# Optimization experiments

Hardware: AMD Instinct MI355X
Metric: run time of the kernel (lower is better)

Reference implementation:

```python
import jax, jax.numpy as jnp
import numpy as np

B, S, H = 1, 2048, 2048
NH, NKV, DH = 8, 1, 256
ROPE_THETA = 10000.0
SCALE = DH ** -0.5
NEG = -1e9


def setup_inputs() -> dict:
    key = jax.random.key(0)
    k1, k2, k3, k4, k5 = jax.random.split(key, 5)
    x = jax.random.normal(k1, (B, S, H), dtype=jnp.float32)
    position_ids = jnp.broadcast_to(jnp.arange(S, dtype=jnp.int32)[None, :], (B, S))
    causal = jnp.tril(jnp.ones((S, S), dtype=bool))
    attention_mask = jnp.where(causal, 0.0, NEG).astype(jnp.float32)[None, None]  # [1,1,S,S]
    std = 0.02
    w_q = jax.random.normal(k2, (H, NH * DH), dtype=jnp.float32) * std
    w_k = jax.random.normal(k3, (H, NKV * DH), dtype=jnp.float32) * std
    w_v = jax.random.normal(k4, (H, NKV * DH), dtype=jnp.float32) * std
    w_o = jax.random.normal(k5, (NH * DH, H), dtype=jnp.float32) * std
    return {"x": x, "position_ids": position_ids, "attention_mask": attention_mask,
            "w_q": w_q, "w_k": w_k, "w_v": w_v, "w_o": w_o}


def _rope_cos_sin(position_ids):
    # inv_freq: [DH/2]
    inv_freq = 1.0 / (ROPE_THETA ** (jnp.arange(0, DH, 2, dtype=jnp.float32) / DH))
    freqs = position_ids.astype(jnp.float32)[:, :, None] * inv_freq[None, None, :]  # [B,S,DH/2]
    emb = jnp.concatenate([freqs, freqs], axis=-1)  # [B,S,DH]
    return jnp.cos(emb), jnp.sin(emb)


def _rotate_half(t):
    t1, t2 = jnp.split(t, 2, axis=-1)
    return jnp.concatenate([-t2, t1], axis=-1)


def reference(x, position_ids, attention_mask, w_q, w_k, w_v, w_o):
    b, s, _ = x.shape
    g = NH // NKV  # kv group size
    q = (x @ w_q).reshape(b, s, NH, DH).transpose(0, 2, 1, 3)   # [b,nh,s,d]
    k = (x @ w_k).reshape(b, s, NKV, DH).transpose(0, 2, 1, 3)  # [b,nkv,s,d]
    v = (x @ w_v).reshape(b, s, NKV, DH).transpose(0, 2, 1, 3)
    cos, sin = _rope_cos_sin(position_ids)
    cos, sin = cos[:, None], sin[:, None]  # broadcast over heads
    q = q * cos + _rotate_half(q) * sin
    k = k * cos + _rotate_half(k) * sin
    # GQA: view q as [b,nkv,g,s,d]; equivalent to repeat_kv without materializing
    qg = q.reshape(b, NKV, g, s, DH)
    scores = jnp.einsum('bkgid,bkjd->bkgij', qg, k) * SCALE      # [b,nkv,g,s,s]
    scores = scores + attention_mask[:, :, None, :, :]
    attn = jax.nn.softmax(scores.astype(jnp.float32), axis=-1).astype(q.dtype)
    out = jnp.einsum('bkgij,bkjd->bkgid', attn, v)               # [b,nkv,g,s,d]
    out = out.reshape(b, NH, s, DH).transpose(0, 2, 1, 3).reshape(b, s, NH * DH)
    out = out @ w_o
    return out, attn.reshape(b, NH, s, s)
```

## Files before the change

kernel.cpp:

```cpp
#include <hip/hip_runtime.h>
#include <hip/hip_bf16.h>
#include <hip/hip_fp16.h>

typedef float f32x4 __attribute__((ext_vector_type(4)));
typedef _Float16 half8 __attribute__((ext_vector_type(8)));
typedef unsigned short u16;
typedef unsigned short u16x8 __attribute__((ext_vector_type(8)));

#define DEVI __device__ __forceinline__

DEVI void async_cp16(void* lds, const void* g) {
  __builtin_amdgcn_global_load_lds(
      (const __attribute__((address_space(1))) void*)g,
      (__attribute__((address_space(3))) void*)lds,
      16, 0, 0);
}

DEVI u16 f2h(float x) {
  union { _Float16 h; u16 u; } v;
  v.h = (_Float16)x;
  return v.u;
}

__global__ __launch_bounds__(256)
void k_prep(const float* __restrict__ x, const float* __restrict__ wq,
            const float* __restrict__ wk, const float* __restrict__ wv,
            const float* __restrict__ wo,
            u16* __restrict__ xb, u16* __restrict__ wqkvT, u16* __restrict__ woT) {
  int bx = blockIdx.x;
  if (bx >= 72) {
    size_t base = ((size_t)(bx - 72) * 32 + blockIdx.y) * 2048 + threadIdx.x * 8;
    float4 v0 = *(const float4*)(x + base);
    float4 v1 = *(const float4*)(x + base + 4);
    ushort4 o0, o1;
    o0.x = f2h(v0.x); o0.y = f2h(v0.y); o0.z = f2h(v0.z); o0.w = f2h(v0.w);
    o1.x = f2h(v1.x); o1.y = f2h(v1.y); o1.z = f2h(v1.z); o1.w = f2h(v1.w);
    *(ushort4*)(xb + base) = o0;
    *(ushort4*)(xb + base + 4) = o1;
    return;
  }
  __shared__ u16 tile[64][65];
  const float* in; int ldin, rowoff, cx; u16* out;
  if (bx < 32)      { in = wq; ldin = 2048; out = wqkvT; rowoff = 0;    cx = bx; }
  else if (bx < 36) { in = wk; ldin = 256;  out = wqkvT; rowoff = 2048; cx = bx - 32; }
  else if (bx < 40) { in = wv; ldin = 256;  out = wqkvT; rowoff = 2304; cx = bx - 36; }
  else              { in = wo; ldin = 2048; out = woT;   rowoff = 0;    cx = bx - 40; }
  int r0 = blockIdx.y * 64, c0 = cx * 64;
  int tx = threadIdx.x & 63, ty = threadIdx.x >> 6;
  for (int rr = ty; rr < 64; rr += 4)
    tile[rr][tx] = f2h(in[(size_t)(r0 + rr) * ldin + (c0 + tx)]);
  __syncthreads();
  for (int rr = ty; rr < 64; rr += 4)
    out[(size_t)(c0 + rr + rowoff) * 2048 + (r0 + tx)] = tile[tx][rr];
}

__global__ __launch_bounds__(256, 2)
void k_gemmQKV(const u16* __restrict__ A, const u16* __restrict__ B,
               const int* __restrict__ pos,
               u16* __restrict__ qh, u16* __restrict__ kh, u16* __restrict__ vT) {
  const int lda = 2048, ldb = 2048;
  const int id = blockIdx.x;
  const int xcd = id & 7, t = id >> 3;
  const int cx = t % 10;
  const int mt = xcd + 8 * (t / 10);
  const int i0 = mt * 64, j0 = cx * 256;

  __shared__ __align__(16) char shm[81920];
  const int tid = threadIdx.x;
  const int wave = tid >> 6, lane = tid & 63;
  const int wn = wave * 64;
  const int quad = lane >> 4, r = lane & 15;

  f32x4 acc[4][4] = {};

  const int srow = tid >> 3;
  const int scol = ((((tid & 7) << 4)) ^ (((tid >> 3) & 7) << 4)) >> 1;
  const u16* gA = A + (size_t)(i0 + srow) * lda + scol;
  const u16* gB = B + (size_t)(j0 + srow) * ldb + scol;
  const int cswz = (quad * 16) ^ ((r & 7) << 4);
  const int nk = 2048 >> 6;

#pragma unroll
  for (int c = 0; c < 2; c++)
    async_cp16(shm + tid * 16 + c * 4096, gA + (size_t)(c * 32) * lda);
#pragma unroll
  for (int c = 0; c < 8; c++)
    async_cp16(shm + 16384 + tid * 16 + c * 4096, gB + (size_t)(c * 32) * ldb);

  for (int kt = 0; kt < nk; kt++) {
    const int cur = kt & 1;
    __builtin_amdgcn_sched_barrier(0);
    asm volatile("s_waitcnt vmcnt(0)" ::: "memory");
    __builtin_amdgcn_s_barrier();
    __builtin_amdgcn_sched_barrier(0);
    if (kt + 1 < nk) {
      const int nxt = cur ^ 1;
      const u16* a1 = gA + (size_t)(kt + 1) * 64;
      const u16* b1 = gB + (size_t)(kt + 1) * 64;
#pragma unroll
      for (int c = 0; c < 2; c++)
        async_cp16(shm + nxt * 8192 + tid * 16 + c * 4096, a1 + (size_t)(c * 32) * lda);
#pragma unroll
      for (int c = 0; c < 8; c++)
        async_cp16(shm + 16384 + nxt * 32768 + tid * 16 + c * 4096, b1 + (size_t)(c * 32) * ldb);
    }
    const char* bufA = shm + cur * 8192;
    const char* bufB = shm + 16384 + cur * 32768;
#pragma unroll
    for (int kh = 0; kh < 2; kh++) {
      const int inrow = cswz ^ (kh * 64);
      half8 af[4], bf[4];
#pragma unroll
      for (int mm = 0; mm < 4; mm++)
        af[mm] = *(const half8*)(bufA + (mm * 16 + r) * 128 + inrow);
#pragma unroll
      for (int n = 0; n < 4; n++)
        bf[n] = *(const half8*)(bufB + (wn + n * 16 + r) * 128 + inrow);
      __builtin_amdgcn_s_setprio(1);
#pragma unroll
      for (int mm = 0; mm < 4; mm++)
#pragma unroll
        for (int n = 0; n < 4; n++)
          acc[mm][n] = __builtin_amdgcn_mfma_f32_16x16x32_f16(af[mm], bf[n], acc[mm][n], 0, 0, 0);
      __builtin_amdgcn_s_setprio(0);
    }
  }

  __syncthreads();
  float* T = (float*)shm;
#pragma unroll
  for (int mm = 0; mm < 4; mm++) {
    int row = mm * 16 + quad * 4;
#pragma unroll
    for (int n = 0; n < 4; n++) {
      int col = wn + n * 16 + r;
#pragma unroll
      for (int v = 0; v < 4; v++) T[(row + v) * 260 + col] = acc[mm][n][v];
    }
  }
  __syncthreads();

  if (cx < 9) {
    const int trow = tid >> 2, tc = tid & 3;
    const int s = i0 + trow;
    u16* dst = (cx < 8) ? (qh + (size_t)s * 2048 + cx * 256) : (kh + (size_t)s * 256);
    const float p = (float)pos[s];
#pragma unroll
    for (int k = 0; k < 4; k++) {
      const int ib = tc * 8 + k * 32;
      u16x8 lo, hi;
#pragma unroll
      for (int e = 0; e < 8; e++) {
        int i = ib + e;
        float fr = __expf((float)i * (-9.210340371976184f / 128.0f)) * p;
        float sn, cs;
        sincosf(fr, &sn, &cs);
        float a = T[trow * 260 + i];
        float b = T[trow * 260 + i + 128];
        lo[e] = f2h(a * cs - b * sn);
        hi[e] = f2h(b * cs + a * sn);
      }
      *(u16x8*)(dst + ib) = lo;
      *(u16x8*)(dst + ib + 128) = hi;
    }
  } else {
    u16* dst = vT + (size_t)tid * 2048 + i0;
#pragma unroll
    for (int c = 0; c < 8; c++) {
      u16x8 w;
#pragma unroll
      for (int e = 0; e < 8; e++) w[e] = f2h(T[(c * 8 + e) * 260 + tid]);
      *(u16x8*)(dst + c * 8) = w;
    }
  }
}

__global__ __launch_bounds__(256, 3)
void k_gemm(const u16* __restrict__ A, int lda,
            const u16* __restrict__ B, int ldb,
            float* __restrict__ C, int ldc, int nN, int K) {
  const int id = blockIdx.x;
  const int xcd = id & 7, t = id >> 3;
  const int by = t % nN;
  const int mt = xcd + 8 * (t / nN);
  const int i0 = mt * 64, j0 = by * 128;

  __shared__ __align__(16) u16 As[2][64 * 64];
  __shared__ __align__(16) u16 Bs[2][128 * 64];
  const int tid = threadIdx.x;
  const int wave = tid >> 6, lane = tid & 63;
  const int wm = (wave >> 1) * 32, wn = (wave & 1) * 64;
  const int quad = lane >> 4, r = lane & 15;

  f32x4 acc[2][4] = {};

  const int srow = tid >> 3;
  const int scol = ((((tid & 7) << 4)) ^ (((tid >> 3) & 7) << 4)) >> 1;
  const u16* gA = A + (size_t)(i0 + srow) * lda + scol;
  const u16* gB = B + (size_t)(j0 + srow) * ldb + scol;
  const int cswz = (quad * 16) ^ ((r & 7) << 4);
  const int nk = K >> 6;

#pragma unroll
  for (int c = 0; c < 2; c++)
    async_cp16((u16*)As[0] + tid * 8 + c * 2048, gA + (size_t)(c * 32) * lda);
#pragma unroll
  for (int c = 0; c < 4; c++)
    async_cp16((u16*)Bs[0] + tid * 8 + c * 2048, gB + (size_t)(c * 32) * ldb);

  for (int kt = 0; kt < nk; kt++) {
    const int cur = kt & 1;
    __builtin_amdgcn_sched_barrier(0);
    asm volatile("s_waitcnt vmcnt(0)" ::: "memory");
    __builtin_amdgcn_s_barrier();
    __builtin_amdgcn_sched_barrier(0);
    if (kt + 1 < nk) {
      const u16* a1 = gA + (size_t)(kt + 1) * 64;
      const u16* b1 = gB + (size_t)(kt + 1) * 64;
#pragma unroll
      for (int c = 0; c < 2; c++)
        async_cp16((u16*)As[cur ^ 1] + tid * 8 + c * 2048, a1 + (size_t)(c * 32) * lda);
#pragma unroll
      for (int c = 0; c < 4; c++)
        async_cp16((u16*)Bs[cur ^ 1] + tid * 8 + c * 2048, b1 + (size_t)(c * 32) * ldb);
    }
    const char* bufA = (const char*)As[cur];
    const char* bufB = (const char*)Bs[cur];
#pragma unroll
    for (int kh = 0; kh < 2; kh++) {
      const int inrow = cswz ^ (kh * 64);
      half8 af[2], bf[4];
#pragma unroll
      for (int mm = 0; mm < 2; mm++)
        af[mm] = *(const half8*)(bufA + (wm + mm * 16 + r) * 128 + inrow);
#pragma unroll
      for (int n = 0; n < 4; n++)
        bf[n] = *(const half8*)(bufB + (wn + n * 16 + r) * 128 + inrow);
      __builtin_amdgcn_s_setprio(1);
#pragma unroll
      for (int mm = 0; mm < 2; mm++)
#pragma unroll
        for (int n = 0; n < 4; n++)
          acc[mm][n] = __builtin_amdgcn_mfma_f32_16x16x32_f16(af[mm], bf[n], acc[mm][n], 0, 0, 0);
      __builtin_amdgcn_s_setprio(0);
    }
  }

#pragma unroll
  for (int mm = 0; mm < 2; mm++) {
    int row = i0 + wm + mm * 16 + quad * 4;
#pragma unroll
    for (int n = 0; n < 4; n++) {
      int col = j0 + wn + n * 16 + r;
      float* cp = C + (size_t)row * ldc + col;
#pragma unroll
      for (int v = 0; v < 4; v++) cp[(size_t)v * ldc] = acc[mm][n][v];
    }
  }
}

__global__ __launch_bounds__(256)
void k_scores(const u16* __restrict__ qh, const u16* __restrict__ kh,
              float* __restrict__ attn, float* __restrict__ lsum) {
  int id = blockIdx.x;
  int ti = (int)((sqrtf(8.0f * (float)id + 1.0f) - 1.0f) * 0.5f);
  while ((ti + 1) * (ti + 2) / 2 <= id) ti++;
  while (ti * (ti + 1) / 2 > id) ti--;
  int tj = id - ti * (ti + 1) / 2;
  const int i0 = ti * 128, j0 = tj * 128;
  const int h = blockIdx.y;
  const int tid = threadIdx.x;
  float* outb = attn + ((size_t)h << 22);

  const u16* A = qh + h * 256;
  __shared__ __align__(16) u16 As[2][128 * 32];
  __shared__ __align__(16) u16 Bs[2][128 * 32];
  __shared__ float psum[128];
  const int wave = tid >> 6, lane = tid & 63;
  const int wm = (wave >> 1) * 64, wn = (wave & 1) * 64;
  const int quad = lane >> 4, r = lane & 15;

  f32x4 acc[4][4] = {};

  const int ar = tid >> 2, ac = (tid & 3) * 8;
  const u16* ag0 = A + (size_t)(i0 + ar) * 2048 + ac;
  const u16* ag1 = ag0 + (size_t)64 * 2048;
  const u16* bg0 = kh + (size_t)(j0 + ar) * 256 + ac;
  const u16* bg1 = bg0 + (size_t)64 * 256;
  const int l0 = tid * 8, l1 = (tid + 256) * 8;

  async_cp16(As[0] + l0, ag0); async_cp16(As[0] + l1, ag1);
  async_cp16(Bs[0] + l0, bg0); async_cp16(Bs[0] + l1, bg1);
  ag0 += 32; ag1 += 32; bg0 += 32; bg1 += 32;
  __syncthreads();

  for (int kt = 0; kt < 8; kt += 2) {
#pragma unroll
    for (int half = 0; half < 2; half++) {
      int cur = half, nxt = half ^ 1;
      if (kt + half + 1 < 8) {
        async_cp16(As[nxt] + l0, ag0); async_cp16(As[nxt] + l1, ag1);
        async_cp16(Bs[nxt] + l0, bg0); async_cp16(Bs[nxt] + l1, bg1);
        ag0 += 32; ag1 += 32; bg0 += 32; bg1 += 32;
      }
      half8 af[4], bf[4];
#pragma unroll
      for (int t = 0; t < 4; t++) af[t] = *(const half8*)(As[cur] + (wm + t * 16 + r) * 32 + quad * 8);
#pragma unroll
      for (int t = 0; t < 4; t++) bf[t] = *(const half8*)(Bs[cur] + (wn + t * 16 + r) * 32 + quad * 8);
#pragma unroll
      for (int ta = 0; ta < 4; ta++)
#pragma unroll
        for (int tb = 0; tb < 4; tb++)
          acc[ta][tb] = __builtin_amdgcn_mfma_f32_16x16x32_f16(af[ta], bf[tb], acc[ta][tb], 0, 0, 0);
      __syncthreads();
    }
  }

  if (tid < 128) psum[tid] = 0.f;
  __syncthreads();
#pragma unroll
  for (int ta = 0; ta < 4; ta++) {
#pragma unroll
    for (int v = 0; v < 4; v++) {
      int row = i0 + wm + ta * 16 + quad * 4 + v;
      float rs = 0.f;
#pragma unroll
      for (int tb = 0; tb < 4; tb++) {
        int col = j0 + wn + tb * 16 + r;
        float val = (col <= row) ? __expf(acc[ta][tb][v] * 0.0625f) : 0.0f;
        outb[(size_t)row * 2048 + col] = val;
        rs += val;
      }
      rs += __shfl_xor(rs, 1); rs += __shfl_xor(rs, 2);
      rs += __shfl_xor(rs, 4); rs += __shfl_xor(rs, 8);
      if (r == 0) atomicAdd(&psum[wm + ta * 16 + quad * 4 + v], rs);
    }
  }
  __syncthreads();
  if (tid < 128)
    lsum[((size_t)h * 2048 + i0 + tid) * 16 + tj] = psum[tid];
}

__global__ __launch_bounds__(256)
void k_pv(float* __restrict__ attn, const u16* __restrict__ vT,
          const float* __restrict__ lsum, u16* __restrict__ o) {
  const int h = blockIdx.y;
  const int i0 = (63 - blockIdx.x) * 32;
  float* Ab = attn + ((size_t)h << 22);
  const int kmax = i0 + 32;
  __shared__ __align__(16) u16 As[2][32 * 64];
  __shared__ __align__(16) u16 Bs[2][256 * 64];
  __shared__ float inv_l[32];
  const int tid = threadIdx.x;
  const int wave = tid >> 6, lane = tid & 63;
  const int wn = wave * 64;
  const int quad = lane >> 4, r = lane & 15;

  if (tid < 32) {
    int i = i0 + tid;
    const float* lp = lsum + ((size_t)h * 2048 + i) * 16;
    int nt = (i >> 7) + 1;
    float s = 0.f;
    for (int t = 0; t < nt; t++) s += lp[t];
    inv_l[tid] = 1.0f / s;
  }
  __syncthreads();

  const int arr = tid >> 3, ac8 = (tid & 7) * 8;
  const int aso = arr * 64 + ((((tid & 7) * 16) ^ ((arr & 7) << 4)) >> 1);
  float* agp = Ab + (size_t)(i0 + arr) * 2048 + ac8;
  const float ainv = inv_l[arr];
  const int brow = tid >> 3;
  const int bcol = ((((tid & 7) * 16)) ^ (((tid >> 3) & 7) << 4)) >> 1;
  const u16* bg = vT + (size_t)brow * 2048 + bcol;
  const int cswz = (quad * 16) ^ ((r & 7) << 4);

  f32x4 acc[2][4] = {};

#define PV_STAGE(buf, k0)                                                        \
  {                                                                              \
    _Pragma("unroll")                                                            \
    for (int c = 0; c < 8; c++)                                                  \
      async_cp16((u16*)Bs[buf] + tid * 8 + c * 2048,                             \
                 bg + (size_t)(c * 32) * 2048 + (k0));                           \
    float4 v0 = *(const float4*)(agp + (k0));                                    \
    float4 v1 = *(const float4*)(agp + (k0) + 4);                                \
    v0.x *= ainv; v0.y *= ainv; v0.z *= ainv; v0.w *= ainv;                      \
    v1.x *= ainv; v1.y *= ainv; v1.z *= ainv; v1.w *= ainv;                      \
    *(float4*)(agp + (k0)) = v0;                                                 \
    *(float4*)(agp + (k0) + 4) = v1;                                             \
    u16x8 w;                                                                     \
    w[0] = f2h(v0.x); w[1] = f2h(v0.y); w[2] = f2h(v0.z); w[3] = f2h(v0.w);      \
    w[4] = f2h(v1.x); w[5] = f2h(v1.y); w[6] = f2h(v1.z); w[7] = f2h(v1.w);      \
    *(u16x8*)((u16*)As[buf] + aso) = w;                                          \
  }

  PV_STAGE(0, 0);
  const int nkt = (kmax + 63) >> 6;
  for (int kt = 0; kt < nkt; kt++) {
    const int cur = kt & 1;
    __syncthreads();
    if (kt + 1 < nkt) PV_STAGE(cur ^ 1, (kt + 1) * 64);
    const char* bA = (const char*)As[cur];
    const char* bB = (const char*)Bs[cur];
#pragma unroll
    for (int kh = 0; kh < 2; kh++) {
      const int inrow = cswz ^ (kh * 64);
      half8 af[2], bf[4];
#pragma unroll
      for (int ta = 0; ta < 2; ta++)
        af[ta] = *(const half8*)(bA + (ta * 16 + r) * 128 + inrow);
#pragma unroll
      for (int tb = 0; tb < 4; tb++)
        bf[tb] = *(const half8*)(bB + (wn + tb * 16 + r) * 128 + inrow);
#pragma unroll
      for (int ta = 0; ta < 2; ta++)
#pragma unroll
        for (int tb = 0; tb < 4; tb++)
          acc[ta][tb] = __builtin_amdgcn_mfma_f32_16x16x32_f16(af[ta], bf[tb], acc[ta][tb], 0, 0, 0);
    }
  }
#pragma unroll
  for (int ta = 0; ta < 2; ta++) {
    int row = i0 + ta * 16 + quad * 4;
#pragma unroll
    for (int tb = 0; tb < 4; tb++) {
      int col = h * 256 + wn + tb * 16 + r;
#pragma unroll
      for (int v = 0; v < 4; v++)
        o[(size_t)(row + v) * 2048 + col] = f2h(acc[ta][tb][v]);
    }
  }
}

extern "C" void kernel_launch(void* const* d_in, const int* in_sizes, int n_in,
                              void* d_out, int out_size, void* d_ws, size_t ws_size,
                              hipStream_t stream) {
  const float* x   = (const float*)d_in[0];
  const int*   pos = (const int*)d_in[1];
  const float* w_q = (const float*)d_in[3];
  const float* w_k = (const float*)d_in[4];
  const float* w_v = (const float*)d_in[5];
  const float* w_o = (const float*)d_in[6];

  float* out  = (float*)d_out;
  float* attn = out + (size_t)2048 * 2048;

  char* ws = (char*)d_ws;
  u16*   xb    = (u16*)ws;
  u16*   wqkvT = xb + (size_t)2048 * 2048;
  u16*   woT   = wqkvT + (size_t)2560 * 2048;
  u16*   qh    = woT + (size_t)2048 * 2048;
  u16*   kh    = qh + (size_t)2048 * 2048;
  u16*   vT    = kh + (size_t)2048 * 256;
  u16*   ob    = vT + (size_t)256 * 2048;
  float* lsum  = (float*)(ob + (size_t)2048 * 2048);

  k_prep<<<dim3(136, 32), 256, 0, stream>>>(x, w_q, w_k, w_v, w_o, xb, wqkvT, woT);

  k_gemmQKV<<<dim3(320), 256, 0, stream>>>(xb, wqkvT, pos, qh, kh, vT);

  k_scores<<<dim3(136, 8), 256, 0, stream>>>(qh, kh, attn, lsum);
  k_pv<<<dim3(64, 8), 256, 0, stream>>>(attn, vT, lsum, ob);

  k_gemm<<<dim3(512), 256, 0, stream>>>(ob, 2048, woT, 2048, out, 2048, 16, 2048);
}
```

Baseline: 326.8 us.

## Fuse scores and PV into one attention kernel keeping probabilities in LDS

Replaces the separate scores kernel (which wrote unnormalised exp to the fp32 attn buffer and partial row sums) and the PV kernel (which re-read, normalised and rewrote attn) with a single kernel per 16-row strip. Each block computes QK^T for its row strip, stores fp16 exponentials in a swizzled 64KB LDS buffer, reduces row sums, then does PV from LDS while writing the normalised attn once. This removes the global round trip of the attention matrix and the lsum buffer. In exchange it uses a fixed exp offset instead of a max subtraction, stores probabilities in fp16, gives small 16-row tiles with K/V loaded directly from global without LDS staging, and the large LDS use limits occupancy.

```diff
diff --git a/kernel.cpp b/kernel.cpp
--- a/kernel.cpp
+++ b/kernel.cpp
@@ -20,6 +20,12 @@
   union { _Float16 h; u16 u; } v;
   v.h = (_Float16)x;
   return v.u;
+}
+
+DEVI float h2f(u16 x) {
+  union { u16 u; _Float16 h; } v;
+  v.u = x;
+  return (float)v.h;
 }
 
 __global__ __launch_bounds__(256)
@@ -107,8 +113,8 @@
     const char* bufA = shm + cur * 8192;
     const char* bufB = shm + 16384 + cur * 32768;
 #pragma unroll
-    for (int kh = 0; kh < 2; kh++) {
-      const int inrow = cswz ^ (kh * 64);
+    for (int kh2 = 0; kh2 < 2; kh2++) {
+      const int inrow = cswz ^ (kh2 * 64);
       half8 af[4], bf[4];
 #pragma unroll
       for (int mm = 0; mm < 4; mm++)
@@ -227,8 +233,8 @@
     const char* bufA = (const char*)As[cur];
     const char* bufB = (const char*)Bs[cur];
 #pragma unroll
-    for (int kh = 0; kh < 2; kh++) {
-      const int inrow = cswz ^ (kh * 64);
+    for (int kh2 = 0; kh2 < 2; kh2++) {
+      const int inrow = cswz ^ (kh2 * 64);
       half8 af[2], bf[4];
 #pragma unroll
       for (int mm = 0; mm < 2; mm++)
@@ -259,177 +265,113 @@
   }
 }
 
-__global__ __launch_bounds__(256)
-void k_scores(const u16* __restrict__ qh, const u16* __restrict__ kh,
-              float* __restrict__ attn, float* __restrict__ lsum) {
-  int id = blockIdx.x;
-  int ti = (int)((sqrtf(8.0f * (float)id + 1.0f) - 1.0f) * 0.5f);
-  while ((ti + 1) * (ti + 2) / 2 <= id) ti++;
-  while (ti * (ti + 1) / 2 > id) ti--;
-  int tj = id - ti * (ti + 1) / 2;
-  const int i0 = ti * 128, j0 = tj * 128;
+__global__ __launch_bounds__(256, 2)
+void k_attn(const u16* __restrict__ qh, const u16* __restrict__ kh,
+            const u16* __restrict__ vT,
+            float* __restrict__ attn, u16* __restrict__ o) {
   const int h = blockIdx.y;
+  const int i0 = (127 - blockIdx.x) * 16;
+  const int kmax = i0 + 16;
+  const int ntiles = (kmax + 127) >> 7;
+
+  __shared__ __align__(16) u16 S16[16 * 2048];
+  __shared__ float rowsum[16];
+  __shared__ float inv_l[16];
+
   const int tid = threadIdx.x;
-  float* outb = attn + ((size_t)h << 22);
-
-  const u16* A = qh + h * 256;
-  __shared__ __align__(16) u16 As[2][128 * 32];
-  __shared__ __align__(16) u16 Bs[2][128 * 32];
-  __shared__ float psum[128];
   const int wave = tid >> 6, lane = tid & 63;
-  const int wm = (wave >> 1) * 64, wn = (wave & 1) * 64;
   const int quad = lane >> 4, r = lane & 15;
 
-  f32x4 acc[4][4] = {};
-
-  const int ar = tid >> 2, ac = (tid & 3) * 8;
-  const u16* ag0 = A + (size_t)(i0 + ar) * 2048 + ac;
-  const u16* ag1 = ag0 + (size_t)64 * 2048;
-  const u16* bg0 = kh + (size_t)(j0 + ar) * 256 + ac;
-  const u16* bg1 = bg0 + (size_t)64 * 256;
-  const int l0 = tid * 8, l1 = (tid + 256) * 8;
-
-  async_cp16(As[0] + l0, ag0); async_cp16(As[0] + l1, ag1);
-  async_cp16(Bs[0] + l0, bg0); async_cp16(Bs[0] + l1, bg1);
-  ag0 += 32; ag1 += 32; bg0 += 32; bg1 += 32;
-  __syncthreads();
-
-  for (int kt = 0; kt < 8; kt += 2) {
-#pragma unroll
-    for (int half = 0; half < 2; half++) {
-      int cur = half, nxt = half ^ 1;
-      if (kt + half + 1 < 8) {
-        async_cp16(As[nxt] + l0, ag0); async_cp16(As[nxt] + l1, ag1);
-        async_cp16(Bs[nxt] + l0, bg0); async_cp16(Bs[nxt] + l1, bg1);
-        ag0 += 32; ag1 += 32; bg0 += 32; bg1 += 32;
-      }
-      half8 af[4], bf[4];
-#pragma unroll
-      for (int t = 0; t < 4; t++) af[t] = *(const half8*)(As[cur] + (wm + t * 16 + r) * 32 + quad * 8);
-#pragma unroll
-      for (int t = 0; t < 4; t++) bf[t] = *(const half8*)(Bs[cur] + (wn + t * 16 + r) * 32 + quad * 8);
-#pragma unroll
-      for (int ta = 0; ta < 4; ta++)
-#pragma unroll
-        for (int tb = 0; tb < 4; tb++)
-          acc[ta][tb] = __builtin_amdgcn_mfma_f32_16x16x32_f16(af[ta], bf[tb], acc[ta][tb], 0, 0, 0);
-      __syncthreads();
-    }
-  }
-
-  if (tid < 128) psum[tid] = 0.f;
-  __syncthreads();
-#pragma unroll
-  for (int ta = 0; ta < 4; ta++) {
+  const u16* qp = qh + (size_t)(i0 + r) * 2048 + h * 256 + quad * 8;
+  half8 qf[8];
+#pragma unroll
+  for (int kf = 0; kf < 8; kf++) qf[kf] = *(const half8*)(qp + kf * 32);
+
+  if (tid < 16) rowsum[tid] = 0.f;
+  __syncthreads();
+
+  for (int jt = 0; jt < ntiles; jt++) {
+    const int jc = jt * 128 + wave * 32;
+    half8 bf[2][8];
+#pragma unroll
+    for (int nf = 0; nf < 2; nf++) {
+      const u16* kp = kh + (size_t)(jc + nf * 16 + r) * 256 + quad * 8;
+#pragma unroll
+      for (int kf = 0; kf < 8; kf++) bf[nf][kf] = *(const half8*)(kp + kf * 32);
+    }
+    f32x4 acc[2] = {};
+#pragma unroll
+    for (int kf = 0; kf < 8; kf++)
+#pragma unroll
+      for (int nf = 0; nf < 2; nf++)
+        acc[nf] = __builtin_amdgcn_mfma_f32_16x16x32_f16(qf[kf], bf[nf][kf], acc[nf], 0, 0, 0);
 #pragma unroll
     for (int v = 0; v < 4; v++) {
-      int row = i0 + wm + ta * 16 + quad * 4 + v;
+      const int row = quad * 4 + v;
+      const int grow = i0 + row;
       float rs = 0.f;
 #pragma unroll
-      for (int tb = 0; tb < 4; tb++) {
-        int col = j0 + wn + tb * 16 + r;
-        float val = (col <= row) ? __expf(acc[ta][tb][v] * 0.0625f) : 0.0f;
-        outb[(size_t)row * 2048 + col] = val;
-        rs += val;
+      for (int nf = 0; nf < 2; nf++) {
+        const int col = jc + nf * 16 + r;
+        float e = (col <= grow) ? __expf(acc[nf][v] * 0.0625f - 4.0f) : 0.f;
+        u16 eh = f2h(e);
+        rs += h2f(eh);
+        S16[row * 2048 + (col ^ ((row & 7) << 3))] = eh;
       }
       rs += __shfl_xor(rs, 1); rs += __shfl_xor(rs, 2);
       rs += __shfl_xor(rs, 4); rs += __shfl_xor(rs, 8);
-      if (r == 0) atomicAdd(&psum[wm + ta * 16 + quad * 4 + v], rs);
-    }
-  }
-  __syncthreads();
-  if (tid < 128)
-    lsum[((size_t)h * 2048 + i0 + tid) * 16 + tj] = psum[tid];
-}
-
-__global__ __launch_bounds__(256)
-void k_pv(float* __restrict__ attn, const u16* __restrict__ vT,
-          const float* __restrict__ lsum, u16* __restrict__ o) {
-  const int h = blockIdx.y;
-  const int i0 = (63 - blockIdx.x) * 32;
-  float* Ab = attn + ((size_t)h << 22);
-  const int kmax = i0 + 32;
-  __shared__ __align__(16) u16 As[2][32 * 64];
-  __shared__ __align__(16) u16 Bs[2][256 * 64];
-  __shared__ float inv_l[32];
-  const int tid = threadIdx.x;
-  const int wave = tid >> 6, lane = tid & 63;
-  const int wn = wave * 64;
-  const int quad = lane >> 4, r = lane & 15;
-
-  if (tid < 32) {
-    int i = i0 + tid;
-    const float* lp = lsum + ((size_t)h * 2048 + i) * 16;
-    int nt = (i >> 7) + 1;
-    float s = 0.f;
-    for (int t = 0; t < nt; t++) s += lp[t];
-    inv_l[tid] = 1.0f / s;
-  }
-  __syncthreads();
-
-  const int arr = tid >> 3, ac8 = (tid & 7) * 8;
-  const int aso = arr * 64 + ((((tid & 7) * 16) ^ ((arr & 7) << 4)) >> 1);
-  float* agp = Ab + (size_t)(i0 + arr) * 2048 + ac8;
-  const float ainv = inv_l[arr];
-  const int brow = tid >> 3;
-  const int bcol = ((((tid & 7) * 16)) ^ (((tid >> 3) & 7) << 4)) >> 1;
-  const u16* bg = vT + (size_t)brow * 2048 + bcol;
-  const int cswz = (quad * 16) ^ ((r & 7) << 4);
-
-  f32x4 acc[2][4] = {};
-
-#define PV_STAGE(buf, k0)                                                        \
-  {                                                                              \
-    _Pragma("unroll")                                                            \
-    for (int c = 0; c < 8; c++)                                                  \
-      async_cp16((u16*)Bs[buf] + tid * 8 + c * 2048,                             \
-                 bg + (size_t)(c * 32) * 2048 + (k0));                           \
-    float4 v0 = *(const float4*)(agp + (k0));                                    \
-    float4 v1 = *(const float4*)(agp + (k0) + 4);                                \
-    v0.x *= ainv; v0.y *= ainv; v0.z *= ainv; v0.w *= ainv;                      \
-    v1.x *= ainv; v1.y *= ainv; v1.z *= ainv; v1.w *= ainv;                      \
-    *(float4*)(agp + (k0)) = v0;                                                 \
-    *(float4*)(agp + (k0) + 4) = v1;                                             \
-    u16x8 w;                                                                     \
-    w[0] = f2h(v0.x); w[1] = f2h(v0.y); w[2] = f2h(v0.z); w[3] = f2h(v0.w);      \
-    w[4] = f2h(v1.x); w[5] = f2h(v1.y); w[6] = f2h(v1.z); w[7] = f2h(v1.w);      \
-    *(u16x8*)((u16*)As[buf] + aso) = w;                                          \
-  }
-
-  PV_STAGE(0, 0);
-  const int nkt = (kmax + 63) >> 6;
-  for (int kt = 0; kt < nkt; kt++) {
-    const int cur = kt & 1;
-    __syncthreads();
-    if (kt + 1 < nkt) PV_STAGE(cur ^ 1, (kt + 1) * 64);
-    const char* bA = (const char*)As[cur];
-    const char* bB = (const char*)Bs[cur];
-#pragma unroll
-    for (int kh = 0; kh < 2; kh++) {
-      const int inrow = cswz ^ (kh * 64);
-      half8 af[2], bf[4];
-#pragma unroll
-      for (int ta = 0; ta < 2; ta++)
-        af[ta] = *(const half8*)(bA + (ta * 16 + r) * 128 + inrow);
-#pragma unroll
-      for (int tb = 0; tb < 4; tb++)
-        bf[tb] = *(const half8*)(bB + (wn + tb * 16 + r) * 128 + inrow);
-#pragma unroll
-      for (int ta = 0; ta < 2; ta++)
-#pragma unroll
-        for (int tb = 0; tb < 4; tb++)
-          acc[ta][tb] = __builtin_amdgcn_mfma_f32_16x16x32_f16(af[ta], bf[tb], acc[ta][tb], 0, 0, 0);
-    }
-  }
-#pragma unroll
-  for (int ta = 0; ta < 2; ta++) {
-    int row = i0 + ta * 16 + quad * 4;
-#pragma unroll
-    for (int tb = 0; tb < 4; tb++) {
-      int col = h * 256 + wn + tb * 16 + r;
-#pragma unroll
-      for (int v = 0; v < 4; v++)
-        o[(size_t)(row + v) * 2048 + col] = f2h(acc[ta][tb][v]);
+      if (r == 0) atomicAdd(&rowsum[row], rs);
+    }
+  }
+  __syncthreads();
+  if (tid < 16) inv_l[tid] = 1.0f / rowsum[tid];
+  __syncthreads();
+
+  const int d0 = wave * 64;
+  const int arow = tid >> 4, acb = (tid & 15) * 8;
+  const float ail = inv_l[arow];
+  float* ap = attn + ((size_t)h << 22) + (size_t)(i0 + arow) * 2048;
+  const u16* sp = S16 + arow * 2048;
+  const int aswz = (arow & 7) << 3;
+
+  f32x4 oacc[4] = {};
+  for (int jt = 0; jt < ntiles; jt++) {
+    half8 pa[4];
+#pragma unroll
+    for (int kf = 0; kf < 4; kf++) {
+      int j = jt * 128 + kf * 32 + quad * 8;
+      pa[kf] = *(const half8*)(S16 + r * 2048 + (j ^ ((r & 7) << 3)));
+    }
+    half8 vf[4][4];
+#pragma unroll
+    for (int nf = 0; nf < 4; nf++) {
+      const u16* vp = vT + (size_t)(d0 + nf * 16 + r) * 2048 + jt * 128 + quad * 8;
+#pragma unroll
+      for (int kf = 0; kf < 4; kf++) vf[nf][kf] = *(const half8*)(vp + kf * 32);
+    }
+#pragma unroll
+    for (int kf = 0; kf < 4; kf++)
+#pragma unroll
+      for (int nf = 0; nf < 4; nf++)
+        oacc[nf] = __builtin_amdgcn_mfma_f32_16x16x32_f16(pa[kf], vf[nf][kf], oacc[nf], 0, 0, 0);
+    const int j = jt * 128 + acb;
+    const u16* s8 = sp + (j ^ aswz);
+    float4 w0, w1;
+    w0.x = h2f(s8[0]) * ail; w0.y = h2f(s8[1]) * ail;
+    w0.z = h2f(s8[2]) * ail; w0.w = h2f(s8[3]) * ail;
+    w1.x = h2f(s8[4]) * ail; w1.y = h2f(s8[5]) * ail;
+    w1.z = h2f(s8[6]) * ail; w1.w = h2f(s8[7]) * ail;
+    *(float4*)(ap + j) = w0;
+    *(float4*)(ap + j + 4) = w1;
+  }
+
+#pragma unroll
+  for (int nf = 0; nf < 4; nf++) {
+#pragma unroll
+    for (int v = 0; v < 4; v++) {
+      const int row = quad * 4 + v;
+      o[(size_t)(i0 + row) * 2048 + h * 256 + d0 + nf * 16 + r] =
+          f2h(oacc[nf][v] * inv_l[row]);
     }
   }
 }
@@ -455,14 +397,12 @@
   u16*   kh    = qh + (size_t)2048 * 2048;
   u16*   vT    = kh + (size_t)2048 * 256;
   u16*   ob    = vT + (size_t)256 * 2048;
-  float* lsum  = (float*)(ob + (size_t)2048 * 2048);
 
   k_prep<<<dim3(136, 32), 256, 0, stream>>>(x, w_q, w_k, w_v, w_o, xb, wqkvT, woT);
 
   k_gemmQKV<<<dim3(320), 256, 0, stream>>>(xb, wqkvT, pos, qh, kh, vT);
 
-  k_scores<<<dim3(136, 8), 256, 0, stream>>>(qh, kh, attn, lsum);
-  k_pv<<<dim3(64, 8), 256, 0, stream>>>(attn, vT, lsum, ob);
+  k_attn<<<dim3(128, 8), 256, 0, stream>>>(qh, kh, vT, attn, ob);
 
   k_gemm<<<dim3(512), 256, 0, stream>>>(ob, 2048, woT, 2048, out, 2048, 16, 2048);
 }
```

Result: slower. 449.8 us (+37.6%).
